# Optimization experiments

Hardware: AMD Instinct MI355X
Metric: run time of the kernel (lower is better)

## Reference

```python
import jax, jax.numpy as jnp
import numpy as np

SLOPE_IN = 0.01  # F.leaky_relu default in the wrapper
SLOPE = 0.2      # DGCNN convention inside EdgeConv blocks
K = 40           # num_points -> k nearest neighbors
LOW = 16         # lowest_size: decoder starting grid
DOM = 128        # domain_size: output grid


def lrelu(x, s):
    return jnp.where(x >= 0, x, s * x)


def conv2d(x, w, b, stride, pad):
    y = jax.lax.conv_general_dilated(x, w, stride, pad,
                                     dimension_numbers=('NCHW', 'OIHW', 'NCHW'))
    return y + b[None, :, None, None]


def knn_idx(x, k):
    # x: (B,C,N) -> (B,N,k) indices of k nearest neighbors (incl. self)
    xx = jnp.sum(x * x, axis=1)                   # (B,N)
    inner = jnp.einsum('bcn,bcm->bnm', x, x)      # (B,N,N)
    neg_d = 2.0 * inner - xx[:, :, None] - xx[:, None, :]
    _, idx = jax.lax.top_k(neg_d, k)
    return idx


def graph_feature(x, idx):
    # x: (B,C,N), idx: (B,N,k) -> (B,2C,N,k): concat(neighbor - center, center)
    nbr = jax.vmap(lambda xf, i: xf[:, i])(x, idx)   # (B,C,N,k)
    ctr = jnp.broadcast_to(x[..., None], nbr.shape)
    return jnp.concatenate([nbr - ctr, ctr], axis=1)


def edge_conv(x, w, b, k):
    # dynamic graph: recompute kNN on current features
    idx = knn_idx(x, k)
    f = graph_feature(x, idx)                                      # (B,2C,N,k)
    h = jnp.einsum('oc,bcnk->bonk', w, f) + b[None, :, None, None]
    return jnp.max(lrelu(h, SLOPE), axis=-1)                       # (B,O,N)


def up2(x):
    return jnp.repeat(jnp.repeat(x, 2, axis=2), 2, axis=3)


def setup_inputs() -> dict:
    key = jax.random.key(0)
    ks = jax.random.split(key, 16)

    def w(k, shape, fan_in):
        return jax.random.normal(k, shape, jnp.float32) / np.float32(np.sqrt(fan_in))

    z = lambda n: jnp.zeros((n,), jnp.float32)
    return {
        'x':  jax.random.normal(ks[0], (2, 10, 2048), jnp.float32),
        'Wc': w(ks[1], (1, 1, 5, 3), 15),      'bc': z(1),
        'W1': w(ks[2], (64, 4), 4),            'b1': z(64),
        'W2': w(ks[3], (64, 128), 128),        'b2': z(64),
        'W3': w(ks[4], (128, 128), 128),       'b3': z(128),
        'W4': w(ks[5], (256, 256), 256),       'b4': z(256),
        'W5': w(ks[6], (1024, 512), 512),      'b5': z(1024),
        'Wfc': w(ks[7], (LOW * LOW * 64, 1024), 1024), 'bfc': z(LOW * LOW * 64),
        'Wd1': w(ks[8], (32, 64, 3, 3), 64 * 9),  'bd1': z(32),
        'Wd2': w(ks[9], (16, 32, 3, 3), 32 * 9),  'bd2': z(16),
        'Wd3': w(ks[10], (1, 16, 3, 3), 16 * 9),  'bd3': z(1),
    }


def reference(x, Wc, bc, W1, b1, W2, b2, W3, b3, W4, b4, W5, b5,
              Wfc, bfc, Wd1, bd1, Wd2, bd2, Wd3, bd3):
    # prefix: conv2d (5,3)/(5,1) + leaky_relu -> (B,1,2,N) -> point coords (B,2,N)
    h = conv2d(x[:, None, :, :], Wc, bc, (5, 1), ((0, 0), (1, 1)))
    h = lrelu(h, SLOPE_IN)[:, 0]                         # (B,2,N)
    # dynamic-graph EdgeConv stack
    x1 = edge_conv(h, W1, b1, K)                         # (B,64,N)
    x2 = edge_conv(x1, W2, b2, K)                        # (B,64,N)
    x3 = edge_conv(x2, W3, b3, K)                        # (B,128,N)
    x4 = edge_conv(x3, W4, b4, K)                        # (B,256,N)
    cat = jnp.concatenate([x1, x2, x3, x4], axis=1)      # (B,512,N)
    g = lrelu(jnp.einsum('oc,bcn->bon', W5, cat) + b5[None, :, None], SLOPE)
    g = jnp.max(g, axis=-1)                              # (B,1024) global feature
    d = lrelu(g @ Wfc.T + bfc, SLOPE).reshape(-1, 64, LOW, LOW)
    d = lrelu(conv2d(up2(d), Wd1, bd1, (1, 1), ((1, 1), (1, 1))), SLOPE)
    d = lrelu(conv2d(up2(d), Wd2, bd2, (1, 1), ((1, 1), (1, 1))), SLOPE)
    d = conv2d(up2(d), Wd3, bd3, (1, 1), ((1, 1), (1, 1)))
    return d
```

## Files before the change

### kernel.cpp

```cpp
#include <hip/hip_runtime.h>
#include <hip/hip_bf16.h>

#define N_PTS 2048
#define BATCH 2
#define KNN 40

typedef __attribute__((ext_vector_type(8))) short bf16x8;
typedef __attribute__((ext_vector_type(16))) float f32x16;

__device__ __forceinline__ float lrelu(float v, float s) {
    return v >= 0.f ? v : s * v;
}

__global__ void prefix_kernel(const float* __restrict__ x, const float* __restrict__ Wc,
                              const float* __restrict__ bc, float* __restrict__ H) {
    int t = blockIdx.x * 256 + threadIdx.x;
    if (t >= BATCH * N_PTS) return;
    int b = t >> 11, n = t & 2047;
    #pragma unroll
    for (int oh = 0; oh < 2; ++oh) {
        float acc = bc[0];
        #pragma unroll
        for (int kh = 0; kh < 5; ++kh) {
            const float* xr = x + ((size_t)b * 10 + oh * 5 + kh) * N_PTS;
            #pragma unroll
            for (int kw = 0; kw < 3; ++kw) {
                int nn = n + kw - 1;
                if (nn >= 0 && nn < N_PTS) acc += xr[nn] * Wc[kh * 3 + kw];
            }
        }
        H[(size_t)t * 2 + oh] = lrelu(acc, 0.01f);
    }
}

__global__ __launch_bounds__(256) void gram_small_kernel(const float* __restrict__ X, long bsX,
                                                         long nstride,
                                                         float* __restrict__ negd) {
    __shared__ float AsT[2][68];
    __shared__ float BsT[2][68];
    __shared__ float xxr[64];
    __shared__ float xxc[64];
    int bz = blockIdx.z;
    const float* Xb = X + (size_t)bz * bsX;
    float* nd = negd + (size_t)bz * nstride;
    int tid = threadIdx.x;
    int r0 = blockIdx.y * 64, c0 = blockIdx.x * 64;
    int ty = tid >> 4, tx = tid & 15;
    if (tid < 128) {
        int r = tid >> 1, c = tid & 1;
        AsT[c][r] = Xb[(size_t)(r0 + r) * 2 + c];
        BsT[c][r] = Xb[(size_t)(c0 + r) * 2 + c];
        int v = (tid < 64) ? (r0 + tid) : (c0 + tid - 64);
        float x0 = Xb[(size_t)v * 2], x1 = Xb[(size_t)v * 2 + 1];
        float s = 0.f;
        s += x0 * x0;
        s += x1 * x1;
        if (tid < 64) xxr[tid] = s; else xxc[tid - 64] = s;
    }
    __syncthreads();
    float acc[4][4] = {};
    #pragma unroll
    for (int k = 0; k < 2; ++k) {
        float4 a = *(const float4*)&AsT[k][ty * 4];
        float4 b = *(const float4*)&BsT[k][tx * 4];
        #pragma unroll
        for (int i = 0; i < 4; ++i)
            #pragma unroll
            for (int j = 0; j < 4; ++j)
                acc[i][j] += (&a.x)[i] * (&b.x)[j];
    }
    #pragma unroll
    for (int i = 0; i < 4; ++i) {
        int r = r0 + ty * 4 + i;
        float xr = xxr[ty * 4 + i];
        #pragma unroll
        for (int j = 0; j < 4; ++j) {
            int c = c0 + tx * 4 + j;
            nd[(size_t)r * N_PTS + c] = 2.0f * acc[i][j] - xr - xxc[tx * 4 + j];
        }
    }
}

template<int C, int STAGE>
__global__ __launch_bounds__(256) void gram_mfma_kernel(
        const short* __restrict__ Xh, const short* __restrict__ Xl, long bsX, int S,
        const float* __restrict__ xx, long xxstride,
        float* __restrict__ negd, long nstride) {
    constexpr int NCH = C / 16;
    __shared__ float xr_s[128];
    __shared__ float xc_s[128];
    int bz = blockIdx.z;
    const short* Ah = Xh + (size_t)bz * bsX;
    const short* Al = Xl + (size_t)bz * bsX;
    const float* xxb = xx + (size_t)bz * xxstride;
    float* nd = negd + (size_t)bz * nstride;
    int tid = threadIdx.x;
    int wave = tid >> 6, lane = tid & 63;
    int wm = wave >> 1, wn = wave & 1;
    int r0 = blockIdx.y * 128 + wm * 64;
    int c0 = blockIdx.x * 128 + wn * 64;
    int rr = lane & 31, kg = lane >> 5;
    if (tid < 128) xr_s[tid] = xxb[blockIdx.y * 128 + tid];
    else           xc_s[tid - 128] = xxb[blockIdx.x * 128 + (tid - 128)];
    const int FS = 32 * S;
    const short* pAh = Ah + (size_t)(r0 + rr) * S + kg * 8;
    const short* pAl = Al + (size_t)(r0 + rr) * S + kg * 8;
    const short* pBh = Ah + (size_t)(c0 + rr) * S + kg * 8;
    const short* pBl = Al + (size_t)(c0 + rr) * S + kg * 8;
    f32x16 a00 = {}, a01 = {}, a10 = {}, a11 = {};
    bf16x8 ah0 = *(const bf16x8*)(pAh);
    bf16x8 ah1 = *(const bf16x8*)(pAh + FS);
    bf16x8 al0 = *(const bf16x8*)(pAl);
    bf16x8 al1 = *(const bf16x8*)(pAl + FS);
    bf16x8 bh0 = *(const bf16x8*)(pBh);
    bf16x8 bh1 = *(const bf16x8*)(pBh + FS);
    bf16x8 bl0 = *(const bf16x8*)(pBl);
    bf16x8 bl1 = *(const bf16x8*)(pBl + FS);
    #pragma unroll 2
    for (int kc = 0; kc < NCH; ++kc) {
        int kn = ((kc + 1) & (NCH - 1)) * 16;
        bf16x8 nah0 = *(const bf16x8*)(pAh + kn);
        bf16x8 nah1 = *(const bf16x8*)(pAh + kn + FS);
        bf16x8 nal0 = *(const bf16x8*)(pAl + kn);
        bf16x8 nal1 = *(const bf16x8*)(pAl + kn + FS);
        bf16x8 nbh0 = *(const bf16x8*)(pBh + kn);
        bf16x8 nbh1 = *(const bf16x8*)(pBh + kn + FS);
        bf16x8 nbl0 = *(const bf16x8*)(pBl + kn);
        bf16x8 nbl1 = *(const bf16x8*)(pBl + kn + FS);
        a00 = __builtin_amdgcn_mfma_f32_32x32x16_bf16(ah0, bh0, a00, 0, 0, 0);
        a00 = __builtin_amdgcn_mfma_f32_32x32x16_bf16(ah0, bl0, a00, 0, 0, 0);
        a00 = __builtin_amdgcn_mfma_f32_32x32x16_bf16(al0, bh0, a00, 0, 0, 0);
        a01 = __builtin_amdgcn_mfma_f32_32x32x16_bf16(ah0, bh1, a01, 0, 0, 0);
        a01 = __builtin_amdgcn_mfma_f32_32x32x16_bf16(ah0, bl1, a01, 0, 0, 0);
        a01 = __builtin_amdgcn_mfma_f32_32x32x16_bf16(al0, bh1, a01, 0, 0, 0);
        a10 = __builtin_amdgcn_mfma_f32_32x32x16_bf16(ah1, bh0, a10, 0, 0, 0);
        a10 = __builtin_amdgcn_mfma_f32_32x32x16_bf16(ah1, bl0, a10, 0, 0, 0);
        a10 = __builtin_amdgcn_mfma_f32_32x32x16_bf16(al1, bh0, a10, 0, 0, 0);
        a11 = __builtin_amdgcn_mfma_f32_32x32x16_bf16(ah1, bh1, a11, 0, 0, 0);
        a11 = __builtin_amdgcn_mfma_f32_32x32x16_bf16(ah1, bl1, a11, 0, 0, 0);
        a11 = __builtin_amdgcn_mfma_f32_32x32x16_bf16(al1, bh1, a11, 0, 0, 0);
        ah0 = nah0; ah1 = nah1; al0 = nal0; al1 = nal1;
        bh0 = nbh0; bh1 = nbh1; bl0 = nbl0; bl1 = nbl1;
    }
    __syncthreads();
    int colF = lane & 31;
    int hi4 = (lane >> 5) * 4;
    #pragma unroll
    for (int f = 0; f < 4; ++f) {
        int fm = f >> 1, fn = f & 1;
        int cIn = wn * 64 + fn * 32 + colF;
        float xc = xc_s[cIn];
        float* ndr = nd + (size_t)(blockIdx.y * 128) * N_PTS + blockIdx.x * 128 + cIn;
        #pragma unroll
        for (int reg = 0; reg < 16; ++reg) {
            float av = (f == 0) ? a00[reg] : (f == 1) ? a01[reg] : (f == 2) ? a10[reg] : a11[reg];
            int rIn = wm * 64 + fm * 32 + (reg & 3) + 8 * (reg >> 2) + hi4;
            ndr[(size_t)rIn * N_PTS] = 2.0f * av - xr_s[rIn] - xc;
        }
    }
}

template<int STAGE>
__global__ __launch_bounds__(256) void topk_kernel(const float* __restrict__ negd, long nstride,
                                                   int* __restrict__ idx_out) {
    __shared__ unsigned hist[2048];
    __shared__ unsigned cand[2048];
    __shared__ unsigned wsum[4];
    __shared__ unsigned sc[4];
    __shared__ unsigned tieb;
    int bz = blockIdx.y;
    int n = blockIdx.x;
    int tid = threadIdx.x;
    int wave = tid >> 6, lane = tid & 63;
    const float* row = negd + (size_t)bz * nstride + (size_t)n * N_PTS;
    float4 v0 = ((const float4*)row)[tid];
    float4 v1 = ((const float4*)row)[tid + 256];
    unsigned k0[4], k1[4];
    #pragma unroll
    for (int e = 0; e < 4; ++e) {
        unsigned u = __float_as_uint((&v0.x)[e]);
        k0[e] = (u & 0x80000000u) ? ~u : (u | 0x80000000u);
        u = __float_as_uint((&v1.x)[e]);
        k1[e] = (u & 0x80000000u) ? ~u : (u | 0x80000000u);
    }
    for (int i = tid; i < 2048; i += 256) hist[i] = 0u;
    if (tid == 0) { sc[2] = 0u; sc[3] = 0u; }
    __syncthreads();
    #pragma unroll
    for (int e = 0; e < 4; ++e) {
        atomicAdd(&hist[k0[e] >> 21], 1u);
        atomicAdd(&hist[k1[e] >> 21], 1u);
    }
    __syncthreads();
    unsigned r = KNN;
    {
        unsigned chunk = 0;
        #pragma unroll
        for (int q = 0; q < 8; ++q) chunk += hist[tid * 8 + q];
        unsigned s = chunk;
        #pragma unroll
        for (int off = 1; off < 64; off <<= 1) {
            unsigned v = __shfl_down(s, off);
            if (lane + off < 64) s += v;
        }
        if (lane == 0) wsum[wave] = s;
        __syncthreads();
        unsigned add = 0;
        for (int w = wave + 1; w < 4; ++w) add += wsum[w];
        unsigned St = s + add, Sn = St - chunk;
        if (St >= r && Sn < r) { sc[0] = (unsigned)tid; sc[1] = r - Sn; }
        __syncthreads();
        if (tid == 0) {
            int c = (int)sc[0]; unsigned rc = sc[1];
            unsigned cum = 0; int b = c * 8 + 7;
            for (;; --b) { cum += hist[b]; if (cum >= rc) break; }
            sc[0] = (unsigned)b; sc[1] = rc - (cum - hist[b]);
        }
        __syncthreads();
    }
    unsigned p1 = sc[0]; r = sc[1];
    __syncthreads();
    for (int i = tid; i < 2048; i += 256) hist[i] = 0u;
    __syncthreads();
    int* out = idx_out + ((size_t)bz * N_PTS + n) * KNN;
    #pragma unroll
    for (int h = 0; h < 2; ++h) {
        #pragma unroll
        for (int e = 0; e < 4; ++e) {
            unsigned u = (h == 0) ? k0[e] : k1[e];
            int j = (tid + h * 256) * 4 + e;
            unsigned b = u >> 21;
            if (b > p1) {
                out[atomicAdd(&sc[2], 1u)] = j;
            } else if (b == p1) {
                unsigned low = u & 0x1FFFFFu;
                cand[atomicAdd(&sc[3], 1u)] = (low << 11) | (unsigned)j;
                atomicAdd(&hist[low >> 10], 1u);
            }
        }
    }
    __syncthreads();
    int cnt = (int)sc[3];
    {
        unsigned chunk = 0;
        #pragma unroll
        for (int q = 0; q < 8; ++q) chunk += hist[tid * 8 + q];
        unsigned s = chunk;
        #pragma unroll
        for (int off = 1; off < 64; off <<= 1) {
            unsigned v = __shfl_down(s, off);
            if (lane + off < 64) s += v;
        }
        if (lane == 0) wsum[wave] = s;
        __syncthreads();
        unsigned add = 0;
        for (int w = wave + 1; w < 4; ++w) add += wsum[w];
        unsigned St = s + add, Sn = St - chunk;
        if (St >= r && Sn < r) { sc[0] = (unsigned)tid; sc[1] = r - Sn; }
        __syncthreads();
        if (tid == 0) {
            int c = (int)sc[0]; unsigned rc = sc[1];
            unsigned cum = 0; int b = c * 8 + 7;
            for (;; --b) { cum += hist[b]; if (cum >= rc) break; }
            sc[0] = (unsigned)b; sc[1] = rc - (cum - hist[b]);
        }
        __syncthreads();
    }
    unsigned b2 = sc[0]; r = sc[1];
    __syncthreads();
    for (int i = tid; i < 1024; i += 256) hist[i] = 0u;
    __syncthreads();
    for (int i = tid; i < cnt; i += 256) {
        unsigned p = cand[i];
        if ((p >> 21) == b2) atomicAdd(&hist[(p >> 11) & 0x3FFu], 1u);
    }
    __syncthreads();
    {
        unsigned chunk = 0;
        #pragma unroll
        for (int q = 0; q < 4; ++q) chunk += hist[tid * 4 + q];
        unsigned s = chunk;
        #pragma unroll
        for (int off = 1; off < 64; off <<= 1) {
            unsigned v = __shfl_down(s, off);
            if (lane + off < 64) s += v;
        }
        if (lane == 0) wsum[wave] = s;
        __syncthreads();
        unsigned add = 0;
        for (int w = wave + 1; w < 4; ++w) add += wsum[w];
        unsigned St = s + add, Sn = St - chunk;
        if (St >= r && Sn < r) { sc[0] = (unsigned)tid; sc[1] = r - Sn; }
        __syncthreads();
        if (tid == 0) {
            int c = (int)sc[0]; unsigned rc = sc[1];
            unsigned cum = 0; int b = c * 4 + 3;
            for (;; --b) { cum += hist[b]; if (cum >= rc) break; }
            sc[0] = (unsigned)b; sc[1] = rc - (cum - hist[b]);
        }
        __syncthreads();
    }
    unsigned Tlow = (b2 << 10) | sc[0];
    unsigned r3 = sc[1];
    __syncthreads();
    for (int i = tid; i < cnt; i += 256) {
        unsigned p = cand[i];
        if ((p >> 11) > Tlow) out[atomicAdd(&sc[2], 1u)] = (int)(p & 0x7FFu);
    }
    __syncthreads();
    int last = -1;
    for (unsigned t = 0; t < r3; ++t) {
        unsigned m = 0xFFFFFFFFu;
        for (int i = tid; i < cnt; i += 256) {
            unsigned p = cand[i];
            if ((p >> 11) == Tlow) {
                int j = (int)(p & 0x7FFu);
                if (j > last && (unsigned)j < m) m = (unsigned)j;
            }
        }
        hist[tid] = m;
        __syncthreads();
        for (int st = 128; st >= 1; st >>= 1) {
            if (tid < st) hist[tid] = min(hist[tid], hist[tid + st]);
            __syncthreads();
        }
        if (tid == 0) { out[KNN - (int)r3 + (int)t] = (int)hist[0]; tieb = hist[0]; }
        __syncthreads();
        last = (int)tieb;
    }
}

template<int C, int O, int STAGE>
__global__ __launch_bounds__(256) void ya_z_kernel(const float* __restrict__ X, int S, long bsX,
                                                   const float* __restrict__ W,
                                                   const float* __restrict__ bias,
                                                   float* __restrict__ YaT, float* __restrict__ ZT) {
    constexpr int KC = (C < 32) ? C : 32;
    __shared__ float Xs[16][KC + 1];
    __shared__ float WaS[KC][64];
    __shared__ float WbS[KC][64];
    int b = blockIdx.z;
    const float* Xb = X + (size_t)b * bsX;
    int n0 = blockIdx.x * 16, o0 = blockIdx.y * 64;
    int tid = threadIdx.x, ty = tid >> 4, tx = tid & 15;
    float aa[4] = {}, ab[4] = {};
    for (int k0 = 0; k0 < C; k0 += KC) {
        __syncthreads();
        for (int i = tid; i < 16 * KC; i += 256) {
            int rw = i / KC, c = i % KC;
            Xs[rw][c] = Xb[(size_t)(n0 + rw) * S + k0 + c];
        }
        for (int i = tid; i < 64 * KC; i += 256) {
            int rw = i / KC, c = i % KC;
            int scol = rw ^ ((c & 15) << 2);
            WaS[c][scol] = W[(size_t)(o0 + rw) * 2 * C + k0 + c];
            WbS[c][scol] = W[(size_t)(o0 + rw) * 2 * C + C + k0 + c];
        }
        __syncthreads();
        #pragma unroll
        for (int k = 0; k < KC; ++k) {
            float xv = Xs[ty][k];
            int m = (k & 15) << 2;
            float4 wa = *(const float4*)&WaS[k][(tx * 4) ^ m];
            float4 wb = *(const float4*)&WbS[k][(tx * 4) ^ m];
            #pragma unroll
            for (int j = 0; j < 4; ++j) {
                aa[j] += xv * (&wa.x)[j];
                ab[j] += xv * (&wb.x)[j];
            }
        }
    }
    int n = n0 + ty;
    float4 ya, zt;
    #pragma unroll
    for (int j = 0; j < 4; ++j) {
        int o = o0 + tx * 4 + j;
        (&ya.x)[j] = aa[j];
        (&zt.x)[j] = ab[j] - aa[j] + bias[o];
    }
    size_t off = ((size_t)b * N_PTS + n) * O + o0 + tx * 4;
    *(float4*)&YaT[off] = ya;
    *(float4*)&ZT[off] = zt;
}

template<int O, int STAGE, int AUX>
__global__ __launch_bounds__(256) void edge_reduce_kernel(const float* __restrict__ YaT,
                                                          const float* __restrict__ ZT,
                                                          const int* __restrict__ IDX,
                                                          float* __restrict__ CATp,
                                                          short* __restrict__ CATh,
                                                          short* __restrict__ CATl,
                                                          float* __restrict__ XX, int coloff) {
    constexpr int TPR = O / 4;
    int b = blockIdx.y;
    int tid = threadIdx.x;
    int n = blockIdx.x * (256 / TPR) + tid / TPR;
    int o = (tid % TPR) * 4;
    const float* Ya_b = YaT + (size_t)b * N_PTS * O;
    size_t rowoff = (size_t)b * N_PTS + n;
    float4 z = *(const float4*)&ZT[rowoff * O + o];
    const int* ir = IDX + rowoff * KNN;
    float4 acc = {-3.4e38f, -3.4e38f, -3.4e38f, -3.4e38f};
    #pragma unroll 8
    for (int k = 0; k < KNN; ++k) {
        int m = ir[k];
        float4 v = *(const float4*)&Ya_b[(size_t)m * O + o];
        acc.x = fmaxf(acc.x, lrelu(v.x + z.x, 0.2f));
        acc.y = fmaxf(acc.y, lrelu(v.y + z.y, 0.2f));
        acc.z = fmaxf(acc.z, lrelu(v.z + z.z, 0.2f));
        acc.w = fmaxf(acc.w, lrelu(v.w + z.w, 0.2f));
    }
    size_t coff = rowoff * 512 + coloff + o;
    *(float4*)&CATp[coff] = acc;
    short4 h, l;
    #pragma unroll
    for (int j = 0; j < 4; ++j) {
        float xv = (&acc.x)[j];
        __hip_bfloat16 hb = __float2bfloat16(xv);
        float hf = __bfloat162float(hb);
        __hip_bfloat16 lb = __float2bfloat16(xv - hf);
        (&h.x)[j] = *reinterpret_cast<short*>(&hb);
        (&l.x)[j] = *reinterpret_cast<short*>(&lb);
    }
    *(short4*)&CATh[coff] = h;
    *(short4*)&CATl[coff] = l;
    if (AUX) {
        float sq = acc.x * acc.x + acc.y * acc.y + acc.z * acc.z + acc.w * acc.w;
        #pragma unroll
        for (int off = 1; off < TPR; off <<= 1) sq += __shfl_xor(sq, off);
        if ((tid % TPR) == 0) XX[rowoff] = sq;
    }
}

__global__ void cvt_split_kernel(const float* __restrict__ src, short* __restrict__ hi,
                                 short* __restrict__ lo, int total4) {
    int t = blockIdx.x * 256 + threadIdx.x;
    if (t >= total4) return;
    float4 v = ((const float4*)src)[t];
    short4 h, l;
    #pragma unroll
    for (int j = 0; j < 4; ++j) {
        float xv = (&v.x)[j];
        __hip_bfloat16 hb = __float2bfloat16(xv);
        float hf = __bfloat162float(hb);
        __hip_bfloat16 lb = __float2bfloat16(xv - hf);
        (&h.x)[j] = *reinterpret_cast<short*>(&hb);
        (&l.x)[j] = *reinterpret_cast<short*>(&lb);
    }
    ((short4*)hi)[t] = h;
    ((short4*)lo)[t] = l;
}

__global__ __launch_bounds__(256) void w5max_mfma_kernel(
        const short* __restrict__ Ah, const short* __restrict__ Al,
        const short* __restrict__ Bh, const short* __restrict__ Bl,
        const float* __restrict__ b5, float* __restrict__ PART) {
    __shared__ float red[2][128];
    int b = blockIdx.z;
    int tid = threadIdx.x;
    int wave = tid >> 6, lane = tid & 63;
    int wm = wave >> 1, wn = wave & 1;
    int m0 = blockIdx.x * 128 + wm * 64;
    int o0 = blockIdx.y * 128 + wn * 64;
    int rr = lane & 31;
    int kg = lane >> 5;
    const int FS = 32 * 512;
    const short* pAh = Ah + ((size_t)b * N_PTS + m0 + rr) * 512 + kg * 8;
    const short* pAl = Al + ((size_t)b * N_PTS + m0 + rr) * 512 + kg * 8;
    const short* pBh = Bh + (size_t)(o0 + rr) * 512 + kg * 8;
    const short* pBl = Bl + (size_t)(o0 + rr) * 512 + kg * 8;
    f32x16 a00 = {}, a01 = {}, a10 = {}, a11 = {};
    bf16x8 ah0 = *(const bf16x8*)(pAh);
    bf16x8 ah1 = *(const bf16x8*)(pAh + FS);
    bf16x8 al0 = *(const bf16x8*)(pAl);
    bf16x8 al1 = *(const bf16x8*)(pAl + FS);
    bf16x8 bh0 = *(const bf16x8*)(pBh);
    bf16x8 bh1 = *(const bf16x8*)(pBh + FS);
    bf16x8 bl0 = *(const bf16x8*)(pBl);
    bf16x8 bl1 = *(const bf16x8*)(pBl + FS);
    #pragma unroll 2
    for (int kc = 0; kc < 32; ++kc) {
        int kn = ((kc + 1) & 31) * 16;
        bf16x8 nah0 = *(const bf16x8*)(pAh + kn);
        bf16x8 nah1 = *(const bf16x8*)(pAh + kn + FS);
        bf16x8 nal0 = *(const bf16x8*)(pAl + kn);
        bf16x8 nal1 = *(const bf16x8*)(pAl + kn + FS);
        bf16x8 nbh0 = *(const bf16x8*)(pBh + kn);
        bf16x8 nbh1 = *(const bf16x8*)(pBh + kn + FS);
        bf16x8 nbl0 = *(const bf16x8*)(pBl + kn);
        bf16x8 nbl1 = *(const bf16x8*)(pBl + kn + FS);
        a00 = __builtin_amdgcn_mfma_f32_32x32x16_bf16(ah0, bh0, a00, 0, 0, 0);
        a00 = __builtin_amdgcn_mfma_f32_32x32x16_bf16(ah0, bl0, a00, 0, 0, 0);
        a00 = __builtin_amdgcn_mfma_f32_32x32x16_bf16(al0, bh0, a00, 0, 0, 0);
        a01 = __builtin_amdgcn_mfma_f32_32x32x16_bf16(ah0, bh1, a01, 0, 0, 0);
        a01 = __builtin_amdgcn_mfma_f32_32x32x16_bf16(ah0, bl1, a01, 0, 0, 0);
        a01 = __builtin_amdgcn_mfma_f32_32x32x16_bf16(al0, bh1, a01, 0, 0, 0);
        a10 = __builtin_amdgcn_mfma_f32_32x32x16_bf16(ah1, bh0, a10, 0, 0, 0);
        a10 = __builtin_amdgcn_mfma_f32_32x32x16_bf16(ah1, bl0, a10, 0, 0, 0);
        a10 = __builtin_amdgcn_mfma_f32_32x32x16_bf16(al1, bh0, a10, 0, 0, 0);
        a11 = __builtin_amdgcn_mfma_f32_32x32x16_bf16(ah1, bh1, a11, 0, 0, 0);
        a11 = __builtin_amdgcn_mfma_f32_32x32x16_bf16(ah1, bl1, a11, 0, 0, 0);
        a11 = __builtin_amdgcn_mfma_f32_32x32x16_bf16(al1, bh1, a11, 0, 0, 0);
        ah0 = nah0; ah1 = nah1; al0 = nal0; al1 = nal1;
        bh0 = nbh0; bh1 = nbh1; bl0 = nbl0; bl1 = nbl1;
    }
    #pragma unroll
    for (int fn = 0; fn < 2; ++fn) {
        float bo = b5[o0 + fn * 32 + rr];
        float m = -3.4e38f;
        #pragma unroll
        for (int r = 0; r < 16; ++r) {
            float v0 = (fn == 0) ? a00[r] : a01[r];
            float v1 = (fn == 0) ? a10[r] : a11[r];
            m = fmaxf(m, lrelu(v0 + bo, 0.2f));
            m = fmaxf(m, lrelu(v1 + bo, 0.2f));
        }
        m = fmaxf(m, __shfl_xor(m, 32));
        red[wm][wn * 64 + fn * 32 + rr] = m;
    }
    __syncthreads();
    if (tid < 128)
        PART[((size_t)b * 16 + blockIdx.x) * 1024 + blockIdx.y * 128 + tid] =
            fmaxf(red[0][tid], red[1][tid]);
}

__global__ void greduce_kernel(const float* __restrict__ PART, float* __restrict__ G) {
    int t = blockIdx.x * 256 + threadIdx.x;
    if (t >= BATCH * 1024) return;
    int b = t >> 10, o = t & 1023;
    const float* p = PART + (size_t)b * 16 * 1024 + o;
    float m = -3.4e38f;
    for (int nb = 0; nb < 16; ++nb) m = fmaxf(m, p[(size_t)nb * 1024]);
    G[t] = m;
}

__global__ __launch_bounds__(256) void fc_kernel(const float* __restrict__ G,
                                                 const float* __restrict__ Wfc,
                                                 const float* __restrict__ bfc,
                                                 float* __restrict__ D0) {
    __shared__ float gl[2][1024];
    int tid = threadIdx.x;
    for (int i = tid; i < 2048; i += 256) gl[i >> 10][i & 1023] = G[i];
    __syncthreads();
    int wave = tid >> 6, lane = tid & 63;
    int j = blockIdx.x * 4 + wave;
    const float* wr = Wfc + (size_t)j * 1024;
    float a0 = 0.f, a1 = 0.f;
    for (int i = lane; i < 1024; i += 64) {
        float w = wr[i];
        a0 += w * gl[0][i];
        a1 += w * gl[1][i];
    }
    #pragma unroll
    for (int off = 32; off; off >>= 1) { a0 += __shfl_xor(a0, off); a1 += __shfl_xor(a1, off); }
    if (lane == 0) {
        float bb = bfc[j];
        D0[j] = lrelu(a0 + bb, 0.2f);
        D0[16384 + j] = lrelu(a1 + bb, 0.2f);
    }
}

template<int CI, int CO, int HI, int WI, int RELU>
__global__ __launch_bounds__(256) void upconv_quad_kernel(const float* __restrict__ in,
                                                          const float* __restrict__ W,
                                                          const float* __restrict__ bias,
                                                          float* __restrict__ out) {
    const int qid = blockIdx.x * 256 + threadIdx.x;
    const int p = qid / WI, q = qid % WI;
    const int co = blockIdx.y, b = blockIdx.z;
    const int HO = HI * 2, WO = WI * 2;
    int off[3][3];
    float msk[3][3];
    #pragma unroll
    for (int r = 0; r < 3; ++r) {
        int pr = p - 1 + r;
        float rm = (pr >= 0 && pr < HI) ? 1.f : 0.f;
        int prc = min(max(pr, 0), HI - 1);
        #pragma unroll
        for (int c = 0; c < 3; ++c) {
            int qc = q - 1 + c;
            float cm = (qc >= 0 && qc < WI) ? 1.f : 0.f;
            int qcc = min(max(qc, 0), WI - 1);
            off[r][c] = prc * WI + qcc;
            msk[r][c] = rm * cm;
        }
    }
    const float* inb = in + (size_t)(b * CI) * HI * WI;
    const float* wco = W + (size_t)co * CI * 9;
    float bb = bias[co];
    float a00 = bb, a01 = bb, a10 = bb, a11 = bb;
    const int me[3] = {0, 1, 1}, mo[3] = {1, 1, 2};
    #pragma unroll 4
    for (int ci = 0; ci < CI; ++ci) {
        const float* ip = inb + (size_t)ci * HI * WI;
        const float* wp = wco + ci * 9;
        float v[3][3];
        #pragma unroll
        for (int r = 0; r < 3; ++r)
            #pragma unroll
            for (int c = 0; c < 3; ++c)
                v[r][c] = msk[r][c] * ip[off[r][c]];
        #pragma unroll
        for (int dy = 0; dy < 3; ++dy) {
            #pragma unroll
            for (int dx = 0; dx < 3; ++dx) {
                float w = wp[dy * 3 + dx];
                a00 += w * v[me[dy]][me[dx]];
                a01 += w * v[me[dy]][mo[dx]];
                a10 += w * v[mo[dy]][me[dx]];
                a11 += w * v[mo[dy]][mo[dx]];
            }
        }
    }
    if (RELU) {
        a00 = lrelu(a00, 0.2f); a01 = lrelu(a01, 0.2f);
        a10 = lrelu(a10, 0.2f); a11 = lrelu(a11, 0.2f);
    }
    float* ob = out + ((size_t)(b * CO + co) * HO + 2 * p) * WO + 2 * q;
    float2 r0 = {a00, a01}, r1 = {a10, a11};
    *(float2*)ob = r0;
    *(float2*)(ob + WO) = r1;
}

extern "C" void kernel_launch(void* const* d_in, const int* in_sizes, int n_in,
                              void* d_out, int out_size, void* d_ws, size_t ws_size,
                              hipStream_t stream) {
    const float* x   = (const float*)d_in[0];
    const float* Wc  = (const float*)d_in[1];
    const float* bc  = (const float*)d_in[2];
    const float* W1  = (const float*)d_in[3];
    const float* b1  = (const float*)d_in[4];
    const float* W2  = (const float*)d_in[5];
    const float* b2  = (const float*)d_in[6];
    const float* W3  = (const float*)d_in[7];
    const float* b3  = (const float*)d_in[8];
    const float* W4  = (const float*)d_in[9];
    const float* b4  = (const float*)d_in[10];
    const float* W5  = (const float*)d_in[11];
    const float* b5  = (const float*)d_in[12];
    const float* Wfc = (const float*)d_in[13];
    const float* bfc = (const float*)d_in[14];
    const float* Wd1 = (const float*)d_in[15];
    const float* bd1 = (const float*)d_in[16];
    const float* Wd2 = (const float*)d_in[17];
    const float* bd2 = (const float*)d_in[18];
    const float* Wd3 = (const float*)d_in[19];
    const float* bd3 = (const float*)d_in[20];
    float* out = (float*)d_out;

    const long NST = (long)N_PTS * N_PTS;
    const size_t TAIL_SZ = 12214272ull;
    const size_t NEED_BATCHED = 16809984ull + 33554432ull + TAIL_SZ;
    const bool batched = ws_size >= NEED_BATCHED;
    const size_t negd_bytes = batched ? 33554432ull : 16777216ull;

    char* ws = (char*)d_ws;
    float* Hb   = (float*)(ws + 0);
    float* CAT  = (float*)(ws + 32768);
    float* YaT  = (float*)(ws + 8421376);
    float* ZT   = (float*)(ws + 12615680);
    float* NEGD = (float*)(ws + 16809984);
    char* tail  = ws + 16809984 + negd_bytes;
    float* XX   = (float*)(tail);
    int*   IDX  = (int*)  (tail + 16384);
    float* PART = (float*)(tail + 671744);
    float* G    = (float*)(tail + 802816);
    float* D0   = (float*)(tail + 811008);
    float* DEC1 = (float*)(tail + 942080);
    float* DEC2 = (float*)(tail + 1204224);
    short* W5h  = (short*)(tail + 1728512);
    short* W5l  = (short*)(tail + 2777088);
    short* CATh = (short*)(tail + 3825664);
    short* CATl = (short*)(tail + 8019968);

    prefix_kernel<<<16, 256, 0, stream>>>(x, Wc, bc, Hb);

    if (batched) {
        gram_small_kernel<<<dim3(32, 32, 2), 256, 0, stream>>>(Hb, (long)N_PTS * 2, NST, NEGD);
        topk_kernel<1><<<dim3(N_PTS, 2), 256, 0, stream>>>(NEGD, NST, IDX);
    } else {
        for (int b = 0; b < BATCH; ++b) {
            gram_small_kernel<<<dim3(32, 32, 1), 256, 0, stream>>>(Hb + (size_t)b * N_PTS * 2, 0,
                                                                   0, NEGD);
            topk_kernel<1><<<dim3(N_PTS, 1), 256, 0, stream>>>(NEGD, 0,
                                                               IDX + (size_t)b * N_PTS * KNN);
        }
    }
    ya_z_kernel<2, 64, 1><<<dim3(128, 1, BATCH), 256, 0, stream>>>(Hb, 2, (long)N_PTS * 2,
                                                                   W1, b1, YaT, ZT);
    edge_reduce_kernel<64, 1, 1><<<dim3(128, BATCH), 256, 0, stream>>>(YaT, ZT, IDX, CAT,
                                                                       CATh, CATl, XX, 0);

    if (batched) {
        gram_mfma_kernel<64, 2><<<dim3(16, 16, 2), 256, 0, stream>>>(
            CATh + 0, CATl + 0, (long)N_PTS * 512, 512, XX, N_PTS, NEGD, NST);
        topk_kernel<2><<<dim3(N_PTS, 2), 256, 0, stream>>>(NEGD, NST, IDX);
    } else {
        for (int b = 0; b < BATCH; ++b) {
            gram_mfma_kernel<64, 2><<<dim3(16, 16, 1), 256, 0, stream>>>(
                CATh + 0 + (size_t)b * N_PTS * 512, CATl + 0 + (size_t)b * N_PTS * 512, 0, 512,
                XX + b * N_PTS, 0, NEGD, 0);
            topk_kernel<2><<<dim3(N_PTS, 1), 256, 0, stream>>>(NEGD, 0,
                                                               IDX + (size_t)b * N_PTS * KNN);
        }
    }
    ya_z_kernel<64, 64, 2><<<dim3(128, 1, BATCH), 256, 0, stream>>>(CAT + 0, 512,
                                                                    (long)N_PTS * 512,
                                                                    W2, b2, YaT, ZT);
    edge_reduce_kernel<64, 2, 1><<<dim3(128, BATCH), 256, 0, stream>>>(YaT, ZT, IDX, CAT,
                                                                       CATh, CATl, XX, 64);

    if (batched) {
        gram_mfma_kernel<64, 3><<<dim3(16, 16, 2), 256, 0, stream>>>(
            CATh + 64, CATl + 64, (long)N_PTS * 512, 512, XX, N_PTS, NEGD, NST);
        topk_kernel<3><<<dim3(N_PTS, 2), 256, 0, stream>>>(NEGD, NST, IDX);
    } else {
        for (int b = 0; b < BATCH; ++b) {
            gram_mfma_kernel<64, 3><<<dim3(16, 16, 1), 256, 0, stream>>>(
                CATh + 64 + (size_t)b * N_PTS * 512, CATl + 64 + (size_t)b * N_PTS * 512, 0, 512,
                XX + b * N_PTS, 0, NEGD, 0);
            topk_kernel<3><<<dim3(N_PTS, 1), 256, 0, stream>>>(NEGD, 0,
                                                               IDX + (size_t)b * N_PTS * KNN);
        }
    }
    ya_z_kernel<64, 128, 3><<<dim3(128, 2, BATCH), 256, 0, stream>>>(CAT + 64, 512,
                                                                     (long)N_PTS * 512,
                                                                     W3, b3, YaT, ZT);
    edge_reduce_kernel<128, 3, 1><<<dim3(256, BATCH), 256, 0, stream>>>(YaT, ZT, IDX, CAT,
                                                                        CATh, CATl, XX, 128);

    if (batched) {
        gram_mfma_kernel<128, 4><<<dim3(16, 16, 2), 256, 0, stream>>>(
            CATh + 128, CATl + 128, (long)N_PTS * 512, 512, XX, N_PTS, NEGD, NST);
        topk_kernel<4><<<dim3(N_PTS, 2), 256, 0, stream>>>(NEGD, NST, IDX);
    } else {
        for (int b = 0; b < BATCH; ++b) {
            gram_mfma_kernel<128, 4><<<dim3(16, 16, 1), 256, 0, stream>>>(
                CATh + 128 + (size_t)b * N_PTS * 512, CATl + 128 + (size_t)b * N_PTS * 512, 0, 512,
                XX + b * N_PTS, 0, NEGD, 0);
            topk_kernel<4><<<dim3(N_PTS, 1), 256, 0, stream>>>(NEGD, 0,
                                                               IDX + (size_t)b * N_PTS * KNN);
        }
    }
    ya_z_kernel<128, 256, 4><<<dim3(128, 4, BATCH), 256, 0, stream>>>(CAT + 128, 512,
                                                                      (long)N_PTS * 512,
                                                                      W4, b4, YaT, ZT);
    edge_reduce_kernel<256, 4, 0><<<dim3(512, BATCH), 256, 0, stream>>>(YaT, ZT, IDX, CAT,
                                                                        CATh, CATl, XX, 256);

    cvt_split_kernel<<<(1024 * 512 / 4 + 255) / 256, 256, 0, stream>>>(
        W5, W5h, W5l, 1024 * 512 / 4);
    w5max_mfma_kernel<<<dim3(16, 8, BATCH), 256, 0, stream>>>(CATh, CATl, W5h, W5l, b5, PART);
    greduce_kernel<<<8, 256, 0, stream>>>(PART, G);
    fc_kernel<<<4096, 256, 0, stream>>>(G, Wfc, bfc, D0);

    upconv_quad_kernel<64, 32, 16, 16, 1><<<dim3(1, 32, BATCH), 256, 0, stream>>>(D0, Wd1, bd1,
                                                                                  DEC1);
    upconv_quad_kernel<32, 16, 32, 32, 1><<<dim3(4, 16, BATCH), 256, 0, stream>>>(DEC1, Wd2, bd2,
                                                                                  DEC2);
    upconv_quad_kernel<16, 1, 64, 64, 0><<<dim3(16, 1, BATCH), 256, 0, stream>>>(DEC2, Wd3, bd3,
                                                                                 out);
}
```

Before: 347.0 us.

## Shrink gram MFMA tile to 64x128 and fuse W5 split into prefix kernel

```diff
diff --git a/kernel.cpp b/kernel.cpp
--- a/kernel.cpp
+++ b/kernel.cpp
@@ -12,9 +12,11 @@
     return v >= 0.f ? v : s * v;
 }
 
-__global__ void prefix_kernel(const float* __restrict__ x, const float* __restrict__ Wc,
-                              const float* __restrict__ bc, float* __restrict__ H) {
-    int t = blockIdx.x * 256 + threadIdx.x;
+__device__ __forceinline__ void prefix_body(int fb, const float* __restrict__ x,
+                                            const float* __restrict__ Wc,
+                                            const float* __restrict__ bc,
+                                            float* __restrict__ H) {
+    int t = fb * 256 + threadIdx.x;
     if (t >= BATCH * N_PTS) return;
     int b = t >> 11, n = t & 2047;
     #pragma unroll
@@ -31,6 +33,37 @@
         }
         H[(size_t)t * 2 + oh] = lrelu(acc, 0.01f);
     }
+}
+
+__device__ __forceinline__ void cvt_body(int t, const float* __restrict__ src,
+                                         short* __restrict__ hi, short* __restrict__ lo,
+                                         int total4) {
+    if (t >= total4) return;
+    float4 v = ((const float4*)src)[t];
+    short4 h, l;
+    #pragma unroll
+    for (int j = 0; j < 4; ++j) {
+        float xv = (&v.x)[j];
+        __hip_bfloat16 hb = __float2bfloat16(xv);
+        float hf = __bfloat162float(hb);
+        __hip_bfloat16 lb = __float2bfloat16(xv - hf);
+        (&h.x)[j] = *reinterpret_cast<short*>(&hb);
+        (&l.x)[j] = *reinterpret_cast<short*>(&lb);
+    }
+    ((short4*)hi)[t] = h;
+    ((short4*)lo)[t] = l;
+}
+
+__global__ __launch_bounds__(256) void prefix_cvt_kernel(const float* __restrict__ x,
+                                                         const float* __restrict__ Wc,
+                                                         const float* __restrict__ bc,
+                                                         float* __restrict__ H,
+                                                         const float* __restrict__ W5,
+                                                         short* __restrict__ W5h,
+                                                         short* __restrict__ W5l) {
+    int fb = blockIdx.x;
+    if (fb < 16) prefix_body(fb, x, Wc, bc, H);
+    else cvt_body((fb - 16) * 256 + threadIdx.x, W5, W5h, W5l, 1024 * 512 / 4);
 }
 
 __global__ __launch_bounds__(256) void gram_small_kernel(const float* __restrict__ X, long bsX,
@@ -87,7 +120,7 @@
         const float* __restrict__ xx, long xxstride,
         float* __restrict__ negd, long nstride) {
     constexpr int NCH = C / 16;
-    __shared__ float xr_s[128];
+    __shared__ float xr_s[64];
     __shared__ float xc_s[128];
     int bz = blockIdx.z;
     const short* Ah = Xh + (size_t)bz * bsX;
@@ -96,67 +129,46 @@
     float* nd = negd + (size_t)bz * nstride;
     int tid = threadIdx.x;
     int wave = tid >> 6, lane = tid & 63;
-    int wm = wave >> 1, wn = wave & 1;
-    int r0 = blockIdx.y * 128 + wm * 64;
-    int c0 = blockIdx.x * 128 + wn * 64;
+    int r0 = blockIdx.y * 64;
+    int c0 = blockIdx.x * 128;
+    int cw = c0 + wave * 32;
     int rr = lane & 31, kg = lane >> 5;
-    if (tid < 128) xr_s[tid] = xxb[blockIdx.y * 128 + tid];
-    else           xc_s[tid - 128] = xxb[blockIdx.x * 128 + (tid - 128)];
+    if (tid < 64) xr_s[tid] = xxb[r0 + tid];
+    else if (tid < 192) xc_s[tid - 64] = xxb[c0 + (tid - 64)];
     const int FS = 32 * S;
     const short* pAh = Ah + (size_t)(r0 + rr) * S + kg * 8;
     const short* pAl = Al + (size_t)(r0 + rr) * S + kg * 8;
-    const short* pBh = Ah + (size_t)(c0 + rr) * S + kg * 8;
-    const short* pBl = Al + (size_t)(c0 + rr) * S + kg * 8;
-    f32x16 a00 = {}, a01 = {}, a10 = {}, a11 = {};
-    bf16x8 ah0 = *(const bf16x8*)(pAh);
-    bf16x8 ah1 = *(const bf16x8*)(pAh + FS);
-    bf16x8 al0 = *(const bf16x8*)(pAl);
-    bf16x8 al1 = *(const bf16x8*)(pAl + FS);
-    bf16x8 bh0 = *(const bf16x8*)(pBh);
-    bf16x8 bh1 = *(const bf16x8*)(pBh + FS);
-    bf16x8 bl0 = *(const bf16x8*)(pBl);
-    bf16x8 bl1 = *(const bf16x8*)(pBl + FS);
+    const short* pBh = Ah + (size_t)(cw + rr) * S + kg * 8;
+    const short* pBl = Al + (size_t)(cw + rr) * S + kg * 8;
+    f32x16 a0 = {}, a1 = {};
     #pragma unroll 2
     for (int kc = 0; kc < NCH; ++kc) {
-        int kn = ((kc + 1) & (NCH - 1)) * 16;
-        bf16x8 nah0 = *(const bf16x8*)(pAh + kn);
-        bf16x8 nah1 = *(const bf16x8*)(pAh + kn + FS);
-        bf16x8 nal0 = *(const bf16x8*)(pAl + kn);
-        bf16x8 nal1 = *(const bf16x8*)(pAl + kn + FS);
-        bf16x8 nbh0 = *(const bf16x8*)(pBh + kn);
-        bf16x8 nbh1 = *(const bf16x8*)(pBh + kn + FS);
-        bf16x8 nbl0 = *(const bf16x8*)(pBl + kn);
-        bf16x8 nbl1 = *(const bf16x8*)(pBl + kn + FS);
-        a00 = __builtin_amdgcn_mfma_f32_32x32x16_bf16(ah0, bh0, a00, 0, 0, 0);
-        a00 = __builtin_amdgcn_mfma_f32_32x32x16_bf16(ah0, bl0, a00, 0, 0, 0);
-        a00 = __builtin_amdgcn_mfma_f32_32x32x16_bf16(al0, bh0, a00, 0, 0, 0);
-        a01 = __builtin_amdgcn_mfma_f32_32x32x16_bf16(ah0, bh1, a01, 0, 0, 0);
-        a01 = __builtin_amdgcn_mfma_f32_32x32x16_bf16(ah0, bl1, a01, 0, 0, 0);
-        a01 = __builtin_amdgcn_mfma_f32_32x32x16_bf16(al0, bh1, a01, 0, 0, 0);
-        a10 = __builtin_amdgcn_mfma_f32_32x32x16_bf16(ah1, bh0, a10, 0, 0, 0);
-        a10 = __builtin_amdgcn_mfma_f32_32x32x16_bf16(ah1, bl0, a10, 0, 0, 0);
-        a10 = __builtin_amdgcn_mfma_f32_32x32x16_bf16(al1, bh0, a10, 0, 0, 0);
-        a11 = __builtin_amdgcn_mfma_f32_32x32x16_bf16(ah1, bh1, a11, 0, 0, 0);
-        a11 = __builtin_amdgcn_mfma_f32_32x32x16_bf16(ah1, bl1, a11, 0, 0, 0);
-        a11 = __builtin_amdgcn_mfma_f32_32x32x16_bf16(al1, bh1, a11, 0, 0, 0);
-        ah0 = nah0; ah1 = nah1; al0 = nal0; al1 = nal1;
-        bh0 = nbh0; bh1 = nbh1; bl0 = nbl0; bl1 = nbl1;
+        int kn = kc * 16;
+        bf16x8 ah0 = *(const bf16x8*)(pAh + kn);
+        bf16x8 ah1 = *(const bf16x8*)(pAh + kn + FS);
+        bf16x8 al0 = *(const bf16x8*)(pAl + kn);
+        bf16x8 al1 = *(const bf16x8*)(pAl + kn + FS);
+        bf16x8 bh = *(const bf16x8*)(pBh + kn);
+        bf16x8 bl = *(const bf16x8*)(pBl + kn);
+        a0 = __builtin_amdgcn_mfma_f32_32x32x16_bf16(ah0, bh, a0, 0, 0, 0);
+        a0 = __builtin_amdgcn_mfma_f32_32x32x16_bf16(ah0, bl, a0, 0, 0, 0);
+        a0 = __builtin_amdgcn_mfma_f32_32x32x16_bf16(al0, bh, a0, 0, 0, 0);
+        a1 = __builtin_amdgcn_mfma_f32_32x32x16_bf16(ah1, bh, a1, 0, 0, 0);
+        a1 = __builtin_amdgcn_mfma_f32_32x32x16_bf16(ah1, bl, a1, 0, 0, 0);
+        a1 = __builtin_amdgcn_mfma_f32_32x32x16_bf16(al1, bh, a1, 0, 0, 0);
     }
     __syncthreads();
     int colF = lane & 31;
     int hi4 = (lane >> 5) * 4;
-    #pragma unroll
-    for (int f = 0; f < 4; ++f) {
-        int fm = f >> 1, fn = f & 1;
-        int cIn = wn * 64 + fn * 32 + colF;
-        float xc = xc_s[cIn];
-        float* ndr = nd + (size_t)(blockIdx.y * 128) * N_PTS + blockIdx.x * 128 + cIn;
-        #pragma unroll
-        for (int reg = 0; reg < 16; ++reg) {
-            float av = (f == 0) ? a00[reg] : (f == 1) ? a01[reg] : (f == 2) ? a10[reg] : a11[reg];
-            int rIn = wm * 64 + fm * 32 + (reg & 3) + 8 * (reg >> 2) + hi4;
-            ndr[(size_t)rIn * N_PTS] = 2.0f * av - xr_s[rIn] - xc;
-        }
+    int cIn = wave * 32 + colF;
+    float xc = xc_s[cIn];
+    float* ndr = nd + (size_t)r0 * N_PTS + c0 + cIn;
+    #pragma unroll
+    for (int reg = 0; reg < 16; ++reg) {
+        int rIn0 = (reg & 3) + 8 * (reg >> 2) + hi4;
+        ndr[(size_t)rIn0 * N_PTS] = 2.0f * a0[reg] - xr_s[rIn0] - xc;
+        int rIn1 = 32 + rIn0;
+        ndr[(size_t)rIn1 * N_PTS] = 2.0f * a1[reg] - xr_s[rIn1] - xc;
     }
 }
 
@@ -430,25 +442,6 @@
         for (int off = 1; off < TPR; off <<= 1) sq += __shfl_xor(sq, off);
         if ((tid % TPR) == 0) XX[rowoff] = sq;
     }
-}
-
-__global__ void cvt_split_kernel(const float* __restrict__ src, short* __restrict__ hi,
-                                 short* __restrict__ lo, int total4) {
-    int t = blockIdx.x * 256 + threadIdx.x;
-    if (t >= total4) return;
-    float4 v = ((const float4*)src)[t];
-    short4 h, l;
-    #pragma unroll
-    for (int j = 0; j < 4; ++j) {
-        float xv = (&v.x)[j];
-        __hip_bfloat16 hb = __float2bfloat16(xv);
-        float hf = __bfloat162float(hb);
-        __hip_bfloat16 lb = __float2bfloat16(xv - hf);
-        (&h.x)[j] = *reinterpret_cast<short*>(&hb);
-        (&l.x)[j] = *reinterpret_cast<short*>(&lb);
-    }
-    ((short4*)hi)[t] = h;
-    ((short4*)lo)[t] = l;
 }
 
 __global__ __launch_bounds__(256) void w5max_mfma_kernel(
@@ -673,11 +666,39 @@
     short* CATh = (short*)(tail + 3825664);
     short* CATl = (short*)(tail + 8019968);
 
-    prefix_kernel<<<16, 256, 0, stream>>>(x, Wc, bc, Hb);
+    prefix_cvt_kernel<<<528, 256, 0, stream>>>(x, Wc, bc, Hb, W5, W5h, W5l);
 
     if (batched) {
         gram_small_kernel<<<dim3(32, 32, 2), 256, 0, stream>>>(Hb, (long)N_PTS * 2, NST, NEGD);
         topk_kernel<1><<<dim3(N_PTS, 2), 256, 0, stream>>>(NEGD, NST, IDX);
+        ya_z_kernel<2, 64, 1><<<dim3(128, 1, BATCH), 256, 0, stream>>>(Hb, 2, (long)N_PTS * 2,
+                                                                       W1, b1, YaT, ZT);
+        edge_reduce_kernel<64, 1, 1><<<dim3(128, BATCH), 256, 0, stream>>>(YaT, ZT, IDX, CAT,
+                                                                           CATh, CATl, XX, 0);
+        gram_mfma_kernel<64, 2><<<dim3(16, 32, 2), 256, 0, stream>>>(
+            CATh + 0, CATl + 0, (long)N_PTS * 512, 512, XX, N_PTS, NEGD, NST);
+        topk_kernel<2><<<dim3(N_PTS, 2), 256, 0, stream>>>(NEGD, NST, IDX);
+        ya_z_kernel<64, 64, 2><<<dim3(128, 1, BATCH), 256, 0, stream>>>(CAT + 0, 512,
+                                                                        (long)N_PTS * 512,
+                                                                        W2, b2, YaT, ZT);
+        edge_reduce_kernel<64, 2, 1><<<dim3(128, BATCH), 256, 0, stream>>>(YaT, ZT, IDX, CAT,
+                                                                           CATh, CATl, XX, 64);
+        gram_mfma_kernel<64, 3><<<dim3(16, 32, 2), 256, 0, stream>>>(
+            CATh + 64, CATl + 64, (long)N_PTS * 512, 512, XX, N_PTS, NEGD, NST);
+        topk_kernel<3><<<dim3(N_PTS, 2), 256, 0, stream>>>(NEGD, NST, IDX);
+        ya_z_kernel<64, 128, 3><<<dim3(128, 2, BATCH), 256, 0, stream>>>(CAT + 64, 512,
+                                                                         (long)N_PTS * 512,
+                                                                         W3, b3, YaT, ZT);
+        edge_reduce_kernel<128, 3, 1><<<dim3(256, BATCH), 256, 0, stream>>>(YaT, ZT, IDX, CAT,
+                                                                            CATh, CATl, XX, 128);
+        gram_mfma_kernel<128, 4><<<dim3(16, 32, 2), 256, 0, stream>>>(
+            CATh + 128, CATl + 128, (long)N_PTS * 512, 512, XX, N_PTS, NEGD, NST);
+        topk_kernel<4><<<dim3(N_PTS, 2), 256, 0, stream>>>(NEGD, NST, IDX);
+        ya_z_kernel<128, 256, 4><<<dim3(128, 4, BATCH), 256, 0, stream>>>(CAT + 128, 512,
+                                                                          (long)N_PTS * 512,
+                                                                          W4, b4, YaT, ZT);
+        edge_reduce_kernel<256, 4, 0><<<dim3(512, BATCH), 256, 0, stream>>>(YaT, ZT, IDX, CAT,
+                                                                            CATh, CATl, XX, 256);
     } else {
         for (int b = 0; b < BATCH; ++b) {
             gram_small_kernel<<<dim3(32, 32, 1), 256, 0, stream>>>(Hb + (size_t)b * N_PTS * 2, 0,
@@ -685,71 +706,48 @@
             topk_kernel<1><<<dim3(N_PTS, 1), 256, 0, stream>>>(NEGD, 0,
                                                                IDX + (size_t)b * N_PTS * KNN);
         }
-    }
-    ya_z_kernel<2, 64, 1><<<dim3(128, 1, BATCH), 256, 0, stream>>>(Hb, 2, (long)N_PTS * 2,
-                                                                   W1, b1, YaT, ZT);
-    edge_reduce_kernel<64, 1, 1><<<dim3(128, BATCH), 256, 0, stream>>>(YaT, ZT, IDX, CAT,
-                                                                       CATh, CATl, XX, 0);
-
-    if (batched) {
-        gram_mfma_kernel<64, 2><<<dim3(16, 16, 2), 256, 0, stream>>>(
-            CATh + 0, CATl + 0, (long)N_PTS * 512, 512, XX, N_PTS, NEGD, NST);
-        topk_kernel<2><<<dim3(N_PTS, 2), 256, 0, stream>>>(NEGD, NST, IDX);
-    } else {
+        ya_z_kernel<2, 64, 1><<<dim3(128, 1, BATCH), 256, 0, stream>>>(Hb, 2, (long)N_PTS * 2,
+                                                                       W1, b1, YaT, ZT);
+        edge_reduce_kernel<64, 1, 1><<<dim3(128, BATCH), 256, 0, stream>>>(YaT, ZT, IDX, CAT,
+                                                                           CATh, CATl, XX, 0);
         for (int b = 0; b < BATCH; ++b) {
-            gram_mfma_kernel<64, 2><<<dim3(16, 16, 1), 256, 0, stream>>>(
+            gram_mfma_kernel<64, 2><<<dim3(16, 32, 1), 256, 0, stream>>>(
                 CATh + 0 + (size_t)b * N_PTS * 512, CATl + 0 + (size_t)b * N_PTS * 512, 0, 512,
                 XX + b * N_PTS, 0, NEGD, 0);
             topk_kernel<2><<<dim3(N_PTS, 1), 256, 0, stream>>>(NEGD, 0,
                                                                IDX + (size_t)b * N_PTS * KNN);
         }
-    }
-    ya_z_kernel<64, 64, 2><<<dim3(128, 1, BATCH), 256, 0, stream>>>(CAT + 0, 512,
-                                                                    (long)N_PTS * 512,
-                                                                    W2, b2, YaT, ZT);
-    edge_reduce_kernel<64, 2, 1><<<dim3(128, BATCH), 256, 0, stream>>>(YaT, ZT, IDX, CAT,
-                                                                       CATh, CATl, XX, 64);
-
-    if (batched) {
-        gram_mfma_kernel<64, 3><<<dim3(16, 16, 2), 256, 0, stream>>>(
-            CATh + 64, CATl + 64, (long)N_PTS * 512, 512, XX, N_PTS, NEGD, NST);
-        topk_kernel<3><<<dim3(N_PTS, 2), 256, 0, stream>>>(NEGD, NST, IDX);
-    } else {
+        ya_z_kernel<64, 64, 2><<<dim3(128, 1, BATCH), 256, 0, stream>>>(CAT + 0, 512,
+                                                                        (long)N_PTS * 512,
+                                                                        W2, b2, YaT, ZT);
+        edge_reduce_kernel<64, 2, 1><<<dim3(128, BATCH), 256, 0, stream>>>(YaT, ZT, IDX, CAT,
+                                                                           CATh, CATl, XX, 64);
         for (int b = 0; b < BATCH; ++b) {
-            gram_mfma_kernel<64, 3><<<dim3(16, 16, 1), 256, 0, stream>>>(
+            gram_mfma_kernel<64, 3><<<dim3(16, 32, 1), 256, 0, stream>>>(
                 CATh + 64 + (size_t)b * N_PTS * 512, CATl + 64 + (size_t)b * N_PTS * 512, 0, 512,
                 XX + b * N_PTS, 0, NEGD, 0);
             topk_kernel<3><<<dim3(N_PTS, 1), 256, 0, stream>>>(NEGD, 0,
                                                                IDX + (size_t)b * N_PTS * KNN);
         }
-    }
-    ya_z_kernel<64, 128, 3><<<dim3(128, 2, BATCH), 256, 0, stream>>>(CAT + 64, 512,
-                                                                     (long)N_PTS * 512,
-                                                                     W3, b3, YaT, ZT);
-    edge_reduce_kernel<128, 3, 1><<<dim3(256, BATCH), 256, 0, stream>>>(YaT, ZT, IDX, CAT,
-                                                                        CATh, CATl, XX, 128);
-
-    if (batched) {
-        gram_mfma_kernel<128, 4><<<dim3(16, 16, 2), 256, 0, stream>>>(
-            CATh + 128, CATl + 128, (long)N_PTS * 512, 512, XX, N_PTS, NEGD, NST);
-        topk_kernel<4><<<dim3(N_PTS, 2), 256, 0, stream>>>(NEGD, NST, IDX);
-    } else {
+        ya_z_kernel<64, 128, 3><<<dim3(128, 2, BATCH), 256, 0, stream>>>(CAT + 64, 512,
+                                                                         (long)N_PTS * 512,
+                                                                         W3, b3, YaT, ZT);
+        edge_reduce_kernel<128, 3, 1><<<dim3(256, BATCH), 256, 0, stream>>>(YaT, ZT, IDX, CAT,
+                                                                            CATh, CATl, XX, 128);
         for (int b = 0; b < BATCH; ++b) {
-            gram_mfma_kernel<128, 4><<<dim3(16, 16, 1), 256, 0, stream>>>(
+            gram_mfma_kernel<128, 4><<<dim3(16, 32, 1), 256, 0, stream>>>(
                 CATh + 128 + (size_t)b * N_PTS * 512, CATl + 128 + (size_t)b * N_PTS * 512, 0, 512,
                 XX + b * N_PTS, 0, NEGD, 0);
             topk_kernel<4><<<dim3(N_PTS, 1), 256, 0, stream>>>(NEGD, 0,
                                                                IDX + (size_t)b * N_PTS * KNN);
         }
-    }
-    ya_z_kernel<128, 256, 4><<<dim3(128, 4, BATCH), 256, 0, stream>>>(CAT + 128, 512,
-                                                                      (long)N_PTS * 512,
-                                                                      W4, b4, YaT, ZT);
-    edge_reduce_kernel<256, 4, 0><<<dim3(512, BATCH), 256, 0, stream>>>(YaT, ZT, IDX, CAT,
-                                                                        CATh, CATl, XX, 256);
-
-    cvt_split_kernel<<<(1024 * 512 / 4 + 255) / 256, 256, 0, stream>>>(
-        W5, W5h, W5l, 1024 * 512 / 4);
+        ya_z_kernel<128, 256, 4><<<dim3(128, 4, BATCH), 256, 0, stream>>>(CAT + 128, 512,
+                                                                          (long)N_PTS * 512,
+                                                                          W4, b4, YaT, ZT);
+        edge_reduce_kernel<256, 4, 0><<<dim3(512, BATCH), 256, 0, stream>>>(YaT, ZT, IDX, CAT,
+                                                                            CATh, CATl, XX, 256);
+    }
+
     w5max_mfma_kernel<<<dim3(16, 8, BATCH), 256, 0, stream>>>(CATh, CATl, W5h, W5l, b5, PART);
     greduce_kernel<<<8, 256, 0, stream>>>(PART, G);
     fc_kernel<<<4096, 256, 0, stream>>>(G, Wfc, bfc, D0);
```

New measurement: 354.3 us (median of 2 runs). 2.1% more time.
